# Performance work log

Hardware: AMD Instinct MI355X
Metric: run time of the kernel (lower is better)

The kernel has to match this reference:

```python
import jax, jax.numpy as jnp
import numpy as np

N_NODES = 8192
N_EDGES = 16384
D = 128          # model_dim
R = 64           # deprel_ext_size
B = 16           # base_size


def setup_inputs() -> dict:
    key = jax.random.key(0)
    k1, k2, k3, k4, k5, k6 = jax.random.split(key, 6)
    inp = jax.random.normal(k1, (N_NODES, D), dtype=jnp.float32)
    deprel_ext_edge = jax.random.randint(k2, (N_EDGES,), 0, R, dtype=jnp.int64)
    edge_index = jax.random.randint(k3, (2, N_EDGES), 0, N_NODES, dtype=jnp.int64)
    # Xavier-uniform-like init scales
    lim_w = float(np.sqrt(6.0 / (D + D)))
    lim_c = float(np.sqrt(6.0 / (R + B)))
    weight = jax.random.uniform(k4, (B, D, D), minval=-lim_w, maxval=lim_w, dtype=jnp.float32)
    w_comp = jax.random.uniform(k5, (R, B), minval=-lim_c, maxval=lim_c, dtype=jnp.float32)
    self_weight = jax.random.uniform(k6, (D, D), minval=-lim_w, maxval=lim_w, dtype=jnp.float32)
    final_bias = jnp.zeros((D,), dtype=jnp.float32)
    return {"inp": inp, "deprel_ext_edge": deprel_ext_edge, "edge_index": edge_index,
            "weight": weight, "w_comp": w_comp, "self_weight": self_weight,
            "final_bias": final_bias}


def reference(inp, deprel_ext_edge, edge_index, weight, w_comp, self_weight, final_bias):
    num_nodes = inp.shape[0]
    # basis decomposition: [R,B] @ [B,D*D] -> [R,D,D]
    full_weight = jnp.einsum('rb,bij->rij', w_comp, weight)
    src = edge_index[0]
    tgt = edge_index[1]
    # per-edge relation weight gather + matvec: [E,D,D], [E,D] -> [E,D]
    filtered_weight = full_weight[deprel_ext_edge]
    filtered_input = inp[src]
    potential_input = jnp.einsum('ei,eij->ej', filtered_input, filtered_weight)
    # neighbor count per (target node, relation) without materializing one-hot:
    # combined index over (node, rel) buckets, segment-sum of ones
    comb = tgt * R + deprel_ext_edge  # [E]
    counts = jax.ops.segment_sum(jnp.ones((comb.shape[0],), dtype=potential_input.dtype),
                                 comb, num_segments=num_nodes * R)
    denumerator = counts[comb][:, None]  # [E,1], always >= 1
    potential_input = potential_input / denumerator
    # scatter-add aggregation into target nodes
    output = jax.ops.segment_sum(potential_input, tgt, num_segments=num_nodes)
    # self-edge projection (nn.Linear: x @ W^T) and final bias
    output = output + inp @ self_weight.T + final_bias
    return output
```

## Files before the change

### kernel.cpp

```cpp
#include <hip/hip_runtime.h>

#define NNODES 8192
#define NEDGES 16384
#define DD 128
#define RR 64
#define BB 16
#define CAP 512
#define ET 11
#define TCAP 20

#define FW_OFF    0
#define RELN_OFF  (FW_OFF + RR*DD*DD)
#define TCNT_OFF  (RELN_OFF + RR)
#define SWT_OFF   (TCNT_OFF + NNODES)
#define SORT_OFF  (SWT_OFF + DD*DD)
#define TLIST_OFF (SORT_OFF + RR*CAP)
#define POT_OFF   (TLIST_OFF + NNODES*TCAP)
#define POTS_OFF  (POT_OFF + NEDGES*DD)

__global__ __launch_bounds__(256) void prep_kernel(
    const float* __restrict__ weight,
    const float* __restrict__ w_comp,
    const float* __restrict__ self_weight,
    const int* __restrict__ deprel,
    const int* __restrict__ edge_index,
    float* __restrict__ ws) {
  const int tid = threadIdx.x, bid = blockIdx.x;
  if (bid < 1024) {
    int r = bid >> 4;
    int ij4 = ((bid & 15) << 8) | tid;
    const float* wc = w_comp + r * BB;
    const float4* w4 = reinterpret_cast<const float4*>(weight);
    float4 acc = {0.f, 0.f, 0.f, 0.f};
#pragma unroll
    for (int b = 0; b < BB; ++b) {
      float c = wc[b];
      float4 v = w4[b * 4096 + ij4];
      acc.x += c * v.x; acc.y += c * v.y; acc.z += c * v.z; acc.w += c * v.w;
    }
    reinterpret_cast<float4*>(ws + FW_OFF)[(r << 12) | ij4] = acc;
  } else if (bid < 1040) {
    int idx = (bid - 1024) * 256 + tid;
    int j = idx >> 5, i0 = (idx & 31) * 4;
    float4 v = *reinterpret_cast<const float4*>(self_weight + j * DD + i0);
    ws[SWT_OFF + (i0 + 0) * DD + j] = v.x;
    ws[SWT_OFF + (i0 + 1) * DD + j] = v.y;
    ws[SWT_OFF + (i0 + 2) * DD + j] = v.z;
    ws[SWT_OFF + (i0 + 3) * DD + j] = v.w;
  } else {
    __shared__ int hist[RR];
    __shared__ int bse[RR];
    int e = (bid - 1040) * 256 + tid;
    int r = deprel[e];
    int t = edge_index[NEDGES + e];
    if (tid < RR) hist[tid] = 0;
    __syncthreads();
    atomicAdd(&hist[r], 1);
    {
      int* tcnt  = reinterpret_cast<int*>(ws + TCNT_OFF);
      int* tlist = reinterpret_cast<int*>(ws + TLIST_OFF);
      int p = atomicAdd(&tcnt[t], 1);
      if (p < TCAP) tlist[t * TCAP + p] = e | (r << 14);
    }
    __syncthreads();
    int* relN = reinterpret_cast<int*>(ws + RELN_OFF);
    if (tid < RR) { bse[tid] = atomicAdd(&relN[tid], hist[tid]); hist[tid] = 0; }
    __syncthreads();
    int p = bse[r] + atomicAdd(&hist[r], 1);
    if (p < CAP) reinterpret_cast<int*>(ws + SORT_OFF)[r * CAP + p] = e;
  }
}

__global__ __launch_bounds__(256, 4) void pot_kernel(
    const float* __restrict__ inp,
    const int* __restrict__ edge_index,
    float* __restrict__ ws) {
  __shared__ __align__(16) float xs[DD * 32];
  __shared__ int eqs[32];
  __shared__ int sqs[32];
  const int tid = threadIdx.x;
  const int* relN  = reinterpret_cast<const int*>(ws + RELN_OFF);
  const int* sortE = reinterpret_cast<const int*>(ws + SORT_OFF);
  float* pot  = ws + POT_OFF;
  float* potS = ws + POTS_OFF;

  const int x = blockIdx.x & 7;
  const int k = blockIdx.x >> 3;
  const bool is_edge = k < 8 * ET;
  int r = 0, base = 0, nrem = 32, n0 = 0;
  const float* wsrc;
  if (is_edge) {
    int q = k / ET;
    r = x + 8 * q;
    base = (k - q * ET) * 32;
    int cnt = min(relN[r], ET * 32);
    if (base >= cnt) return;
    nrem = min(32, cnt - base);
    wsrc = ws + FW_OFF + r * DD * DD;
  } else {
    n0 = (x * 32 + (k - 8 * ET)) * 32;
    wsrc = ws + SWT_OFF;
  }

  if (tid < 32) {
    int e = 0, s = 0;
    if (is_edge) {
      if (tid < nrem) {
        e = sortE[r * CAP + base + tid];
        s = edge_index[e];
      }
    } else { s = n0 + tid; }
    eqs[tid] = e; sqs[tid] = s;
  }
  __syncthreads();

  {
    int m = tid & 31, ih = tid >> 5;
    int s = sqs[m];
    const float4* srcp = reinterpret_cast<const float4*>(inp + s * DD + ih * 16);
#pragma unroll
    for (int kk = 0; kk < 4; ++kk) {
      float4 v = srcp[kk];
      int i = ih * 16 + kk * 4;
      xs[(i + 0) * 32 + m] = v.x;
      xs[(i + 1) * 32 + m] = v.y;
      xs[(i + 2) * 32 + m] = v.z;
      xs[(i + 3) * 32 + m] = v.w;
    }
  }
  __syncthreads();

  const int jq = tid & 31, mg = tid >> 5;
  const int j0 = jq * 4, m0 = mg * 4;
  float acc[4][4] = {};
#pragma unroll 16
  for (int i = 0; i < DD; ++i) {
    float4 x4 = *reinterpret_cast<const float4*>(&xs[i * 32 + m0]);
    float4 w4 = *reinterpret_cast<const float4*>(wsrc + i * DD + j0);
    acc[0][0] += x4.x * w4.x; acc[0][1] += x4.x * w4.y; acc[0][2] += x4.x * w4.z; acc[0][3] += x4.x * w4.w;
    acc[1][0] += x4.y * w4.x; acc[1][1] += x4.y * w4.y; acc[1][2] += x4.y * w4.z; acc[1][3] += x4.y * w4.w;
    acc[2][0] += x4.z * w4.x; acc[2][1] += x4.z * w4.y; acc[2][2] += x4.z * w4.z; acc[2][3] += x4.z * w4.w;
    acc[3][0] += x4.w * w4.x; acc[3][1] += x4.w * w4.y; acc[3][2] += x4.w * w4.z; acc[3][3] += x4.w * w4.w;
  }

  if (is_edge) {
#pragma unroll
    for (int mi = 0; mi < 4; ++mi) {
      int mm = m0 + mi;
      if (mm < nrem) {
        float4 o = {acc[mi][0], acc[mi][1], acc[mi][2], acc[mi][3]};
        *reinterpret_cast<float4*>(pot + eqs[mm] * DD + j0) = o;
      }
    }
  } else {
#pragma unroll
    for (int mi = 0; mi < 4; ++mi) {
      float4 o = {acc[mi][0], acc[mi][1], acc[mi][2], acc[mi][3]};
      *reinterpret_cast<float4*>(potS + (n0 + m0 + mi) * DD + j0) = o;
    }
  }
}

__global__ __launch_bounds__(256) void gather_kernel(
    const float* __restrict__ bias,
    const float* __restrict__ ws,
    float* __restrict__ out) {
  const int tid = threadIdx.x;
  const int t = blockIdx.x * 8 + (tid >> 5);
  const int j0 = (tid & 31) * 4;
  const int* tcnt = reinterpret_cast<const int*>(ws + TCNT_OFF);
  const int* tl   = reinterpret_cast<const int*>(ws + TLIST_OFF) + t * TCAP;
  const float* pot  = ws + POT_OFF;
  const float* potS = ws + POTS_OFF;

  float4 s = *reinterpret_cast<const float4*>(potS + t * DD + j0);
  float4 b4 = *reinterpret_cast<const float4*>(bias + j0);
  s.x += b4.x; s.y += b4.y; s.z += b4.z; s.w += b4.w;

  int deg = min(tcnt[t], TCAP);
  for (int d = 0; d < deg; ++d) {
    int pk = tl[d];
    int e = pk & 16383, rl = pk >> 14;
    int c = 0;
    for (int d2 = 0; d2 < deg; ++d2) c += ((tl[d2] >> 14) == rl);
    float sc = 1.0f / (float)c;
    float4 p = *reinterpret_cast<const float4*>(pot + e * DD + j0);
    s.x += p.x * sc; s.y += p.y * sc; s.z += p.z * sc; s.w += p.w * sc;
  }
  *reinterpret_cast<float4*>(out + t * DD + j0) = s;
}

extern "C" void kernel_launch(void* const* d_in, const int* in_sizes, int n_in,
                              void* d_out, int out_size, void* d_ws, size_t ws_size,
                              hipStream_t stream) {
  const float* inp        = (const float*)d_in[0];
  const int*   deprel     = (const int*)d_in[1];
  const int*   edge_index = (const int*)d_in[2];
  const float* weight     = (const float*)d_in[3];
  const float* w_comp     = (const float*)d_in[4];
  const float* self_w     = (const float*)d_in[5];
  const float* bias       = (const float*)d_in[6];
  float* out = (float*)d_out;
  float* ws  = (float*)d_ws;

  hipMemsetAsync(ws + RELN_OFF, 0, (size_t)(RR + NNODES) * sizeof(float), stream);
  prep_kernel<<<1104, 256, 0, stream>>>(weight, w_comp, self_w, deprel, edge_index, ws);
  pot_kernel<<<8 * (8 * ET + 32), 256, 0, stream>>>(inp, edge_index, ws);
  gather_kernel<<<NNODES / 8, 256, 0, stream>>>(bias, ws, out);
}
```

Baseline: 108.8 us.

## Bucket edges in two single-block shared-memory passes and drop the memset launch

Edge bucketing by relation and by target node now runs in two dedicated blocks that use shared-memory atomics and then write out the counts. This removes the separate hipMemsetAsync and the global atomics spread over 64 blocks. pot_kernel and gather_kernel get higher occupancy hints and pot's unroll is halved. The risk is that the two serial blocks, each looping over all 16K edges, lengthen the prep kernel's critical path, and the higher occupancy hint may cause register spills.

```diff
diff --git a/kernel.cpp b/kernel.cpp
--- a/kernel.cpp
+++ b/kernel.cpp
@@ -8,6 +8,7 @@
 #define CAP 512
 #define ET 11
 #define TCAP 20
+#define POTTASKS (8 * (8 * ET + 32))
 
 #define FW_OFF    0
 #define RELN_OFF  (FW_OFF + RR*DD*DD)
@@ -25,10 +26,41 @@
     const int* __restrict__ deprel,
     const int* __restrict__ edge_index,
     float* __restrict__ ws) {
+  __shared__ int lbuf[NNODES];
+  __shared__ int lrn[RR];
   const int tid = threadIdx.x, bid = blockIdx.x;
-  if (bid < 1024) {
-    int r = bid >> 4;
-    int ij4 = ((bid & 15) << 8) | tid;
+  if (bid == 0) {
+    if (tid < RR) lrn[tid] = 0;
+    __syncthreads();
+    int* sortE = reinterpret_cast<int*>(ws + SORT_OFF);
+#pragma unroll 4
+    for (int it = 0; it < NEDGES / 256; ++it) {
+      int e = it * 256 + tid;
+      int r = deprel[e];
+      int p = atomicAdd(&lrn[r], 1);
+      if (p < CAP) sortE[r * CAP + p] = e;
+    }
+    __syncthreads();
+    if (tid < RR) reinterpret_cast<int*>(ws + RELN_OFF)[tid] = lrn[tid];
+  } else if (bid == 1) {
+    for (int i = tid; i < NNODES; i += 256) lbuf[i] = 0;
+    __syncthreads();
+    int* tlist = reinterpret_cast<int*>(ws + TLIST_OFF);
+#pragma unroll 4
+    for (int it = 0; it < NEDGES / 256; ++it) {
+      int e = it * 256 + tid;
+      int r = deprel[e];
+      int t = edge_index[NEDGES + e];
+      int q = atomicAdd(&lbuf[t], 1);
+      if (q < TCAP) tlist[t * TCAP + q] = e | (r << 14);
+    }
+    __syncthreads();
+    for (int i = tid; i < NNODES; i += 256)
+      reinterpret_cast<int*>(ws + TCNT_OFF)[i] = lbuf[i];
+  } else if (bid < 1026) {
+    int g = bid - 2;
+    int r = g >> 4;
+    int ij4 = ((g & 15) << 8) | tid;
     const float* wc = w_comp + r * BB;
     const float4* w4 = reinterpret_cast<const float4*>(weight);
     float4 acc = {0.f, 0.f, 0.f, 0.f};
@@ -39,39 +71,18 @@
       acc.x += c * v.x; acc.y += c * v.y; acc.z += c * v.z; acc.w += c * v.w;
     }
     reinterpret_cast<float4*>(ws + FW_OFF)[(r << 12) | ij4] = acc;
-  } else if (bid < 1040) {
-    int idx = (bid - 1024) * 256 + tid;
+  } else {
+    int idx = (bid - 1026) * 256 + tid;
     int j = idx >> 5, i0 = (idx & 31) * 4;
     float4 v = *reinterpret_cast<const float4*>(self_weight + j * DD + i0);
     ws[SWT_OFF + (i0 + 0) * DD + j] = v.x;
     ws[SWT_OFF + (i0 + 1) * DD + j] = v.y;
     ws[SWT_OFF + (i0 + 2) * DD + j] = v.z;
     ws[SWT_OFF + (i0 + 3) * DD + j] = v.w;
-  } else {
-    __shared__ int hist[RR];
-    __shared__ int bse[RR];
-    int e = (bid - 1040) * 256 + tid;
-    int r = deprel[e];
-    int t = edge_index[NEDGES + e];
-    if (tid < RR) hist[tid] = 0;
-    __syncthreads();
-    atomicAdd(&hist[r], 1);
-    {
-      int* tcnt  = reinterpret_cast<int*>(ws + TCNT_OFF);
-      int* tlist = reinterpret_cast<int*>(ws + TLIST_OFF);
-      int p = atomicAdd(&tcnt[t], 1);
-      if (p < TCAP) tlist[t * TCAP + p] = e | (r << 14);
-    }
-    __syncthreads();
-    int* relN = reinterpret_cast<int*>(ws + RELN_OFF);
-    if (tid < RR) { bse[tid] = atomicAdd(&relN[tid], hist[tid]); hist[tid] = 0; }
-    __syncthreads();
-    int p = bse[r] + atomicAdd(&hist[r], 1);
-    if (p < CAP) reinterpret_cast<int*>(ws + SORT_OFF)[r * CAP + p] = e;
-  }
-}
-
-__global__ __launch_bounds__(256, 4) void pot_kernel(
+  }
+}
+
+__global__ __launch_bounds__(256, 8) void pot_kernel(
     const float* __restrict__ inp,
     const int* __restrict__ edge_index,
     float* __restrict__ ws) {
@@ -133,7 +144,7 @@
   const int jq = tid & 31, mg = tid >> 5;
   const int j0 = jq * 4, m0 = mg * 4;
   float acc[4][4] = {};
-#pragma unroll 16
+#pragma unroll 8
   for (int i = 0; i < DD; ++i) {
     float4 x4 = *reinterpret_cast<const float4*>(&xs[i * 32 + m0]);
     float4 w4 = *reinterpret_cast<const float4*>(wsrc + i * DD + j0);
@@ -161,7 +172,7 @@
   }
 }
 
-__global__ __launch_bounds__(256) void gather_kernel(
+__global__ __launch_bounds__(256, 8) void gather_kernel(
     const float* __restrict__ bias,
     const float* __restrict__ ws,
     float* __restrict__ out) {
@@ -203,8 +214,7 @@
   float* out = (float*)d_out;
   float* ws  = (float*)d_ws;
 
-  hipMemsetAsync(ws + RELN_OFF, 0, (size_t)(RR + NNODES) * sizeof(float), stream);
-  prep_kernel<<<1104, 256, 0, stream>>>(weight, w_comp, self_w, deprel, edge_index, ws);
-  pot_kernel<<<8 * (8 * ET + 32), 256, 0, stream>>>(inp, edge_index, ws);
+  prep_kernel<<<1042, 256, 0, stream>>>(weight, w_comp, self_w, deprel, edge_index, ws);
+  pot_kernel<<<POTTASKS, 256, 0, stream>>>(inp, edge_index, ws);
   gather_kernel<<<NNODES / 8, 256, 0, stream>>>(bias, ws, out);
 }
```

Result: slower. 145.7 us (+33.9%).
